# Kernel tuning notes

Hardware: AMD Instinct MI355X
Metric: run time of the kernel (lower is better)

## Reference

```python
import jax, jax.numpy as jnp
import numpy as np

B, H, W = 8, 160, 160
L = H * W  # 25600, matches nn.LayerNorm(25600)
QDIM = KDIM = MID = OUT = 256
HEADS = 8
HEAD_DIM = MID // HEADS  # 32
LN_EPS = 1e-5


def conv1x1(x, w, b):
    # x: [N,C,H,W], w: [O,C], b: [O] -> [N,O,H,W]
    return jnp.einsum('nchw,oc->nohw', x, w) + b[None, :, None, None]


def setup_inputs() -> dict:
    key = jax.random.key(0)
    ks = jax.random.split(key, 12)
    s = 0.02
    return {
        'query': jax.random.normal(ks[0], (B, QDIM, H, W), jnp.float32),
        'key': jax.random.normal(ks[1], (B, KDIM, H, W), jnp.float32),
        'Wq': jax.random.normal(ks[2], (MID, QDIM), jnp.float32) * s,
        'bq': jnp.zeros((MID,), jnp.float32),
        'Wk': jax.random.normal(ks[3], (MID, KDIM), jnp.float32) * s,
        'bk': jnp.zeros((MID,), jnp.float32),
        'Wv': jax.random.normal(ks[4], (MID, KDIM), jnp.float32) * s,
        'bv': jnp.zeros((MID,), jnp.float32),
        'Wo': jax.random.normal(ks[5], (OUT, MID), jnp.float32) * s,
        'bo': jnp.zeros((OUT,), jnp.float32),
        'gamma': jnp.ones((L,), jnp.float32),
        'beta': jnp.zeros((L,), jnp.float32),
    }


def reference(query, key, Wq, bq, Wk, bk, Wv, bv, Wo, bo, gamma, beta):
    # 1x1-conv projections, flatten spatial dims to L
    q = conv1x1(query, Wq, bq).reshape(B, HEADS, HEAD_DIM, L)
    k = conv1x1(key, Wk, bk).reshape(B, HEADS, HEAD_DIM, L)
    v = conv1x1(key, Wv, bv).reshape(B, HEADS, HEAD_DIM, L)
    # NOTE: faithful to the source, scores contract over L (spatial), giving
    # a [B, heads, head_dim, head_dim] channel-attention matrix.
    scores = jnp.einsum('nhdl,nhel->nhde', q, k) / (KDIM ** 0.5)
    attn = jax.nn.softmax(scores, axis=-1)  # dropout is identity at eval
    out = jnp.einsum('nhde,nhel->nhdl', attn, v).reshape(B, MID, L)
    # LayerNorm over the flattened spatial axis (size 25600)
    mu = jnp.mean(out, axis=-1, keepdims=True)
    var = jnp.var(out, axis=-1, keepdims=True)
    out = (out - mu) * jax.lax.rsqrt(var + LN_EPS) * gamma + beta
    out = out.reshape(B, MID, H, W)
    return conv1x1(out, Wo, bo)
```

## Files before the change

### kernel.cpp

```cpp
#include <hip/hip_runtime.h>
#include <hip/hip_bf16.h>
#include <stdint.h>

#define LROW 25600
#define NCH 256
#define LN_EPS 1e-5f

typedef float f32x4 __attribute__((ext_vector_type(4)));
typedef __bf16 bf16x8 __attribute__((ext_vector_type(8)));

__device__ __forceinline__ bf16x8 cvt8(f32x4 a, f32x4 b) {
  bf16x8 r;
  r[0] = (__bf16)a[0]; r[1] = (__bf16)a[1]; r[2] = (__bf16)a[2]; r[3] = (__bf16)a[3];
  r[4] = (__bf16)b[0]; r[5] = (__bf16)b[1]; r[6] = (__bf16)b[2]; r[7] = (__bf16)b[3];
  return r;
}

__device__ __forceinline__ void wg_bar() {
  asm volatile("s_waitcnt lgkmcnt(0)\n\ts_barrier" ::: "memory");
}

__global__ __launch_bounds__(1024, 4) void gram_k(
    const float* __restrict__ qg, const float* __restrict__ kg,
    float* __restrict__ Gd, float* __restrict__ Gkkd,
    float* __restrict__ sq, float* __restrict__ sk) {
  __shared__ __align__(16) __bf16 lA[256 * 32];
  __shared__ __align__(16) __bf16 lB[256 * 32];

  const int bid = blockIdx.x;
  const int x = bid & 7;
  int n = bid >> 3;
  int b = 0, s = 0;
  for (int bb = 0; bb < 8; ++bb) {
    const int gsl = (x - bb) & 7;
    const int gs = (21 * gsl + 7) >> 3, ge = (21 * gsl + 28) >> 3;
    const int ks = (11 * gsl + 7) >> 3, ke = (11 * gsl + 18) >> 3;
    const int cnt = (ge - gs) + (ke - ks);
    if (n < cnt) {
      b = bb;
      s = (n < ge - gs) ? (gs + n) : (21 + ks + (n - (ge - gs)));
      break;
    }
    n -= cnt;
  }

  const int mat = (s < 21) ? 0 : 1;
  const int idx = mat ? (s - 21) : s;
  const int parts = mat ? 11 : 21;
  const int c0 = (800 * idx) / parts, c1 = (800 * (idx + 1)) / parts;
  const int nc = c1 - c0;
  const int tid = threadIdx.x;
  const int w = tid >> 6, lane = tid & 63;
  const int wr = w >> 2, wc = w & 3;
  const int lr = lane & 15, g = lane >> 4;
  const float* Ag = (mat ? kg : qg) + (size_t)b * NCH * LROW;
  const float* Bg = kg + (size_t)b * NCH * LROW;

  const int rowS = tid >> 2, uS = tid & 3;
  const int uSw = uS ^ ((rowS >> 1) & 3);
  const size_t gOff = (size_t)rowS * LROW + uS * 8;
  __bf16* ldsA_dst = lA + rowS * 32 + uSw * 8;
  __bf16* ldsB_dst = lB + rowS * 32 + uSw * 8;

  const f32x4 zero = {0.f, 0.f, 0.f, 0.f};
  f32x4 acc[4][4];
#pragma unroll
  for (int i = 0; i < 4; ++i)
#pragma unroll
    for (int j = 0; j < 4; ++j) acc[i][j] = zero;

  float rsum = 0.f;

  auto LOADG = [&](int c, f32x4* d) {
    const float* pa = Ag + gOff + (size_t)c * 32;
    d[0] = *(const f32x4*)pa;
    d[1] = *(const f32x4*)(pa + 4);
    if (mat == 0) {
      const float* pb = Bg + gOff + (size_t)c * 32;
      d[2] = *(const f32x4*)pb;
      d[3] = *(const f32x4*)(pb + 4);
    }
  };

  auto PROCESS = [&](f32x4* d) {
#pragma unroll
    for (int e = 0; e < 4; ++e) rsum += d[0][e] + d[1][e];
    *(bf16x8*)ldsA_dst = cvt8(d[0], d[1]);
    if (mat == 0) *(bf16x8*)ldsB_dst = cvt8(d[2], d[3]);
    wg_bar();
    const __bf16* Bp = mat ? lA : lB;
    bf16x8 af[4];
#pragma unroll
    for (int i = 0; i < 4; ++i) {
      const int row = wr * 64 + i * 16 + lr;
      const int u = g ^ ((row >> 1) & 3);
      af[i] = *(const bf16x8*)(lA + row * 32 + u * 8);
    }
#pragma unroll
    for (int j = 0; j < 4; ++j) {
      const int row = wc * 64 + j * 16 + lr;
      const int u = g ^ ((row >> 1) & 3);
      bf16x8 bfj = *(const bf16x8*)(Bp + row * 32 + u * 8);
#pragma unroll
      for (int i = 0; i < 4; ++i)
        acc[i][j] = __builtin_amdgcn_mfma_f32_16x16x32_bf16(af[i], bfj, acc[i][j], 0, 0, 0);
    }
    wg_bar();
  };

  f32x4 bA[4], bB[4];
  LOADG(c0, bA);
  int cc = 0;
  for (; cc + 2 <= nc; cc += 2) {
    LOADG(c0 + cc + 1, bB);
    PROCESS(bA);
    if (cc + 2 < nc) LOADG(c0 + cc + 2, bA);
    PROCESS(bB);
  }
  if (cc < nc) PROCESS(bA);

  atomicAdd((mat ? sk : sq) + b * NCH + rowS, rsum);

  float* Gout = (mat ? Gkkd : Gd) + (size_t)b * 65536;
#pragma unroll
  for (int i = 0; i < 4; ++i)
#pragma unroll
    for (int j = 0; j < 4; ++j) {
      const int col = wc * 64 + j * 16 + lr;
      const int row0 = wr * 64 + i * 16 + g * 4;
#pragma unroll
      for (int r = 0; r < 4; ++r)
        atomicAdd(&Gout[(size_t)(row0 + r) * NCH + col], acc[i][j][r]);
    }
}

__global__ __launch_bounds__(256) void attn_k(
    const float* __restrict__ G, const float* __restrict__ sq,
    const float* __restrict__ sk,
    const float* __restrict__ Wq, const float* __restrict__ bq,
    const float* __restrict__ Wk, const float* __restrict__ bk,
    const float* __restrict__ Wv, const float* __restrict__ bv,
    float* __restrict__ M, float* __restrict__ cvec) {
  __shared__ float Wql[32][257];
  __shared__ float Wkl[32][257];
  __shared__ float QGl[32][257];
  __shared__ float Sl[32][33];
  __shared__ float Al[32][33];
  __shared__ float ul[32], wl[32];
  const int b = blockIdx.x >> 3, h = blockIdx.x & 7;
  const int t = threadIdx.x;
  const float* Gb = G + (size_t)b * 65536;

  for (int i = 0; i < 32; ++i) {
    int idx = i * 256 + t;
    int d = idx >> 8, c = idx & 255;
    Wql[d][c] = Wq[(h * 32 + d) * 256 + c];
    Wkl[d][c] = Wk[(h * 32 + d) * 256 + c];
  }
  __syncthreads();
  {
    float a[32];
#pragma unroll
    for (int d = 0; d < 32; ++d) a[d] = 0.f;
    for (int c = 0; c < 256; ++c) {
      float gv = Gb[c * 256 + t];
#pragma unroll
      for (int d = 0; d < 32; ++d) a[d] += Wql[d][c] * gv;
    }
    for (int d = 0; d < 32; ++d) QGl[d][t] = a[d];
  }
  if (t < 32) {
    float u = 0.f, wv = 0.f;
    for (int c = 0; c < 256; ++c) {
      u += Wql[t][c] * sq[b * 256 + c];
      wv += Wkl[t][c] * sk[b * 256 + c];
    }
    ul[t] = u; wl[t] = wv;
  }
  __syncthreads();
  for (int i = 0; i < 4; ++i) {
    int idx = i * 256 + t;
    int d = idx >> 5, e = idx & 31;
    float sv = 0.f;
    for (int c = 0; c < 256; ++c) sv += QGl[d][c] * Wkl[e][c];
    float bqd = bq[h * 32 + d], bke = bk[h * 32 + e];
    Sl[d][e] = (sv + ul[d] * bke + bqd * wl[e] + 25600.f * bqd * bke) * (1.f / 16.f);
  }
  __syncthreads();
  if (t < 32) {
    float m = -1e30f;
    for (int e = 0; e < 32; ++e) m = fmaxf(m, Sl[t][e]);
    float ssum = 0.f;
    for (int e = 0; e < 32; ++e) { float p = __expf(Sl[t][e] - m); Al[t][e] = p; ssum += p; }
    float is = 1.f / ssum;
    for (int e = 0; e < 32; ++e) Al[t][e] *= is;
  }
  __syncthreads();
  {
    float a[32];
#pragma unroll
    for (int d = 0; d < 32; ++d) a[d] = 0.f;
    for (int e = 0; e < 32; ++e) {
      float wv = Wv[(h * 32 + e) * 256 + t];
#pragma unroll
      for (int d = 0; d < 32; ++d) a[d] += Al[d][e] * wv;
    }
    for (int d = 0; d < 32; ++d) M[((size_t)b * 256 + h * 32 + d) * 256 + t] = a[d];
  }
  if (t < 32) {
    float cv = 0.f;
    for (int e = 0; e < 32; ++e) cv += Al[t][e] * bv[h * 32 + e];
    cvec[b * 256 + h * 32 + t] = cv;
  }
}

__global__ __launch_bounds__(256) void stats_k(
    const float* __restrict__ Gkk, const float* __restrict__ M,
    const float* __restrict__ sk, const float* __restrict__ cvec,
    float* __restrict__ mu, float* __restrict__ inv) {
  __shared__ float Ml[32][257];
  __shared__ float Ql[32][257];
  const int b = blockIdx.x >> 3, cb = blockIdx.x & 7;
  const int t = threadIdx.x;
  const float* Gk = Gkk + (size_t)b * 65536;
  for (int i = 0; i < 32; ++i) {
    int idx = i * 256 + t;
    Ml[idx >> 8][idx & 255] = M[((size_t)b * 256 + cb * 32 + (idx >> 8)) * 256 + (idx & 255)];
  }
  __syncthreads();
  {
    float a[32];
#pragma unroll
    for (int c = 0; c < 32; ++c) a[c] = 0.f;
    for (int cc = 0; cc < 256; ++cc) {
      float gv = Gk[cc * 256 + t];
#pragma unroll
      for (int c = 0; c < 32; ++c) a[c] += Ml[c][cc] * gv;
    }
    for (int c = 0; c < 32; ++c) Ql[c][t] = a[c];
  }
  __syncthreads();
  if (t < 32) {
    float qf = 0.f, msk = 0.f;
    for (int j = 0; j < 256; ++j) {
      qf += Ql[t][j] * Ml[t][j];
      msk += Ml[t][j] * sk[b * 256 + j];
    }
    int c = cb * 32 + t;
    float cv = cvec[b * 256 + c];
    float muv = msk * (1.f / 25600.f) + cv;
    float sum2 = qf + 2.f * cv * msk + 25600.f * cv * cv;
    float var = sum2 * (1.f / 25600.f) - muv * muv;
    mu[b * 256 + c] = muv;
    inv[b * 256 + c] = rsqrtf(var + LN_EPS);
  }
}

__global__ __launch_bounds__(256) void pmat_k(
    const float* __restrict__ M, const float* __restrict__ Wo,
    const float* __restrict__ inv, const float* __restrict__ cvec,
    const float* __restrict__ mu, __bf16* __restrict__ Pb,
    float* __restrict__ t1, float* __restrict__ wsum) {
  __shared__ float Wol[32][257];
  __shared__ float invl[256];
  const int b = blockIdx.x >> 3, ob = blockIdx.x & 7;
  const int t = threadIdx.x;
  invl[t] = inv[b * 256 + t];
  __syncthreads();
  for (int i = 0; i < 32; ++i) {
    int idx = i * 256 + t;
    int o = idx >> 8, c = idx & 255;
    Wol[o][c] = Wo[(ob * 32 + o) * 256 + c] * invl[c];
  }
  __syncthreads();
  {
    float a[32];
#pragma unroll
    for (int o = 0; o < 32; ++o) a[o] = 0.f;
    for (int c = 0; c < 256; ++c) {
      float m = M[((size_t)b * 256 + c) * 256 + t];
#pragma unroll
      for (int o = 0; o < 32; ++o) a[o] += Wol[o][c] * m;
    }
    for (int o = 0; o < 32; ++o)
      Pb[((size_t)b * 256 + ob * 32 + o) * 256 + t] = (__bf16)a[o];
  }
  if (t < 32) {
    float s1 = 0.f, s2 = 0.f;
    for (int c = 0; c < 256; ++c) {
      s1 += Wol[t][c] * (cvec[b * 256 + c] - mu[b * 256 + c]);
      s2 += Wo[(ob * 32 + t) * 256 + c];
    }
    t1[b * 256 + ob * 32 + t] = s1;
    wsum[b * 256 + ob * 32 + t] = s2;
  }
}

__global__ __launch_bounds__(512, 4) void outf_k(
    const float* __restrict__ key, const __bf16* __restrict__ Pb,
    const float* __restrict__ t1, const float* __restrict__ wsum,
    const float* __restrict__ bo, const float* __restrict__ gamma,
    const float* __restrict__ beta, float* __restrict__ out) {
  __shared__ __align__(16) __bf16 Bt[128 * 256];
  const int bid = blockIdx.x;
  const int b = bid / 200, lt = bid % 200, l0 = lt * 128;
  const int tid = threadIdx.x, w = tid >> 6, lane = tid & 63;
  const int wr = w >> 1, wc = w & 1;
  const int lr = lane & 15, g = lane >> 4;
  const float* Kb = key + (size_t)b * NCH * LROW;

  {
    const int c = tid & 255, seg = tid >> 8;
    const int uc = c >> 3, cb2 = (c & 7) * 2;
    const float* src = Kb + (size_t)c * LROW + l0 + seg * 64;
#pragma unroll
    for (int i = 0; i < 16; ++i) {
      f32x4 v = *(const f32x4*)(src + i * 4);
#pragma unroll
      for (int j = 0; j < 4; ++j) {
        const int l = seg * 64 + i * 4 + j;
        *(__bf16*)((char*)Bt + l * 512 + ((uc ^ (l & 7)) << 4) + cb2) = (__bf16)v[j];
      }
    }
  }
  __syncthreads();

  const f32x4 zero = {0.f, 0.f, 0.f, 0.f};
  f32x4 acc[4][4];
#pragma unroll
  for (int i = 0; i < 4; ++i)
#pragma unroll
    for (int j = 0; j < 4; ++j) acc[i][j] = zero;

  const __bf16* Pbase = Pb + (size_t)b * 65536;
#pragma unroll
  for (int ks = 0; ks < 8; ++ks) {
    bf16x8 af[4];
#pragma unroll
    for (int i = 0; i < 4; ++i) {
      const int row = wr * 64 + i * 16 + lr;
      af[i] = *(const bf16x8*)(Pbase + (size_t)row * 256 + ks * 32 + g * 8);
    }
#pragma unroll
    for (int j = 0; j < 4; ++j) {
      const int col = wc * 64 + j * 16 + lr;
      const int unit = ks * 4 + g;
      bf16x8 bfj = *(const bf16x8*)((const char*)Bt + col * 512 + ((unit ^ (col & 7)) << 4));
#pragma unroll
      for (int i = 0; i < 4; ++i)
        acc[i][j] = __builtin_amdgcn_mfma_f32_16x16x32_bf16(af[i], bfj, acc[i][j], 0, 0, 0);
    }
  }

  float t1r[4][4], wsr[4][4], bor[4][4];
#pragma unroll
  for (int i = 0; i < 4; ++i)
#pragma unroll
    for (int r = 0; r < 4; ++r) {
      const int row = wr * 64 + i * 16 + g * 4 + r;
      t1r[i][r] = t1[b * 256 + row];
      wsr[i][r] = wsum[b * 256 + row];
      bor[i][r] = bo[row];
    }
#pragma unroll
  for (int j = 0; j < 4; ++j) {
    const int colg = l0 + wc * 64 + j * 16 + lr;
    const float gm = gamma[colg];
    const float bt = beta[colg];
#pragma unroll
    for (int i = 0; i < 4; ++i) {
      const int row0 = wr * 64 + i * 16 + g * 4;
#pragma unroll
      for (int r = 0; r < 4; ++r) {
        const int row = row0 + r;
        float v = gm * (acc[i][j][r] + t1r[i][r]) + bt * wsr[i][r] + bor[i][r];
        out[((size_t)b * 256 + row) * LROW + colg] = v;
      }
    }
  }
}

extern "C" void kernel_launch(void* const* d_in, const int* in_sizes, int n_in,
                              void* d_out, int out_size, void* d_ws, size_t ws_size,
                              hipStream_t stream) {
  const float* query = (const float*)d_in[0];
  const float* key   = (const float*)d_in[1];
  const float* Wq = (const float*)d_in[2];
  const float* bq = (const float*)d_in[3];
  const float* Wk = (const float*)d_in[4];
  const float* bk = (const float*)d_in[5];
  const float* Wv = (const float*)d_in[6];
  const float* bv = (const float*)d_in[7];
  const float* Wo = (const float*)d_in[8];
  const float* bo = (const float*)d_in[9];
  const float* gamma = (const float*)d_in[10];
  const float* beta  = (const float*)d_in[11];
  float* out = (float*)d_out;

  float* ws = (float*)d_ws;
  float* G    = ws;
  float* Gkk  = G + 524288;
  float* sq   = Gkk + 524288;
  float* sk   = sq + 2048;
  float* M    = sk + 2048;
  float* cvec = M + 524288;
  float* mu   = cvec + 2048;
  float* inv  = mu + 2048;
  float* t1   = inv + 2048;
  float* wsum = t1 + 2048;
  __bf16* Pb  = (__bf16*)(wsum + 2048);

  hipMemsetAsync(d_ws, 0, (size_t)(524288 * 2 + 4096) * sizeof(float), stream);

  gram_k<<<256, 1024, 0, stream>>>(query, key, G, Gkk, sq, sk);
  attn_k<<<64, 256, 0, stream>>>(G, sq, sk, Wq, bq, Wk, bk, Wv, bv, M, cvec);
  stats_k<<<64, 256, 0, stream>>>(Gkk, M, sk, cvec, mu, inv);
  pmat_k<<<64, 256, 0, stream>>>(M, Wo, inv, cvec, mu, Pb, t1, wsum);
  outf_k<<<1600, 512, 0, stream>>>(key, Pb, t1, wsum, bo, gamma, beta, out);
}
```

Measured before the change: 707.1 us.

## Retile Gram kernel into 128x128 double-buffered tiles with split-K partials and reduction

Changes the Gram computation from 256 blocks of 1024 threads covering a full 256x256 tile to 768 blocks of 256 threads. Each block computes a 128x128 quadrant over one of 12 K-slices and double-buffers shared memory, which removes one barrier per step. When the workspace is large enough, partial Gram matrices are written out plainly and summed by a new reduce kernel, replacing the global float atomics. It also adds unroll pragmas to the small attention and stats kernels, reorders the output kernel's block-to-batch mapping, and restructures its epilogue. In exchange the partial buffers cost extra memory traffic, and the Kkt Gram is now computed in full rather than reusing the symmetric load.

Result: slower. 1.032 ms (+46.0%).

```diff
diff --git a/kernel.cpp b/kernel.cpp
--- a/kernel.cpp
+++ b/kernel.cpp
@@ -20,47 +20,39 @@
   asm volatile("s_waitcnt lgkmcnt(0)\n\ts_barrier" ::: "memory");
 }
 
-__global__ __launch_bounds__(1024, 4) void gram_k(
+template <int FULL>
+__global__ __launch_bounds__(256, 3) void gram_k(
     const float* __restrict__ qg, const float* __restrict__ kg,
-    float* __restrict__ Gd, float* __restrict__ Gkkd,
+    float* __restrict__ P0,
+    float* __restrict__ P1,
     float* __restrict__ sq, float* __restrict__ sk) {
-  __shared__ __align__(16) __bf16 lA[256 * 32];
-  __shared__ __align__(16) __bf16 lB[256 * 32];
+  __shared__ __align__(16) __bf16 lA[2][128 * 32];
+  __shared__ __align__(16) __bf16 lB[2][128 * 32];
 
   const int bid = blockIdx.x;
-  const int x = bid & 7;
-  int n = bid >> 3;
-  int b = 0, s = 0;
-  for (int bb = 0; bb < 8; ++bb) {
-    const int gsl = (x - bb) & 7;
-    const int gs = (21 * gsl + 7) >> 3, ge = (21 * gsl + 28) >> 3;
-    const int ks = (11 * gsl + 7) >> 3, ke = (11 * gsl + 18) >> 3;
-    const int cnt = (ge - gs) + (ke - ks);
-    if (n < cnt) {
-      b = bb;
-      s = (n < ge - gs) ? (gs + n) : (21 + ks + (n - (ge - gs)));
-      break;
-    }
-    n -= cnt;
-  }
-
-  const int mat = (s < 21) ? 0 : 1;
-  const int idx = mat ? (s - 21) : s;
-  const int parts = mat ? 11 : 21;
-  const int c0 = (800 * idx) / parts, c1 = (800 * (idx + 1)) / parts;
+  const int xcd = bid & 7, s2 = bid >> 3;
+  const int tile = s2 & 7, gslot = s2 >> 3;
+  const int g = gslot * 8 + xcd;
+  const int b = g / 12, ks = g % 12;
+  const int mat = tile >> 2;
+  const int ri = (tile >> 1) & 1, ci = tile & 1;
+  const int c0 = (800 * ks) / 12, c1 = (800 * (ks + 1)) / 12;
   const int nc = c1 - c0;
+
   const int tid = threadIdx.x;
   const int w = tid >> 6, lane = tid & 63;
-  const int wr = w >> 2, wc = w & 3;
-  const int lr = lane & 15, g = lane >> 4;
-  const float* Ag = (mat ? kg : qg) + (size_t)b * NCH * LROW;
-  const float* Bg = kg + (size_t)b * NCH * LROW;
-
-  const int rowS = tid >> 2, uS = tid & 3;
-  const int uSw = uS ^ ((rowS >> 1) & 3);
-  const size_t gOff = (size_t)rowS * LROW + uS * 8;
-  __bf16* ldsA_dst = lA + rowS * 32 + uSw * 8;
-  __bf16* ldsB_dst = lB + rowS * 32 + uSw * 8;
+  const int wr = w >> 1, wc = w & 1;
+  const int lr = lane & 15, gq = lane >> 4;
+
+  const float* Abase = (mat ? kg : qg) + (size_t)b * NCH * LROW + (size_t)(ri * 128) * LROW;
+  const float* Bbase = kg + (size_t)b * NCH * LROW + (size_t)(ci * 128) * LROW;
+
+  const int rowS = tid >> 1, h = tid & 1;
+  const float* Ap = Abase + (size_t)rowS * LROW + h * 16 + (size_t)c0 * 32;
+  const float* Bp = Bbase + (size_t)rowS * LROW + h * 16 + (size_t)c0 * 32;
+  const int swz = rowS & 3;
+  const int d0 = rowS * 32 + (((2 * h) ^ swz) * 8);
+  const int d1 = rowS * 32 + (((2 * h + 1) ^ swz) * 8);
 
   const f32x4 zero = {0.f, 0.f, 0.f, 0.f};
   f32x4 acc[4][4];
@@ -70,68 +62,101 @@
     for (int j = 0; j < 4; ++j) acc[i][j] = zero;
 
   float rsum = 0.f;
+  f32x4 bA[8], bB[8];
 
   auto LOADG = [&](int c, f32x4* d) {
-    const float* pa = Ag + gOff + (size_t)c * 32;
-    d[0] = *(const f32x4*)pa;
-    d[1] = *(const f32x4*)(pa + 4);
-    if (mat == 0) {
-      const float* pb = Bg + gOff + (size_t)c * 32;
-      d[2] = *(const f32x4*)pb;
-      d[3] = *(const f32x4*)(pb + 4);
-    }
+    const float* pa = Ap + (size_t)c * 32;
+#pragma unroll
+    for (int i = 0; i < 4; ++i) d[i] = *(const f32x4*)(pa + i * 4);
+    const float* pb = Bp + (size_t)c * 32;
+#pragma unroll
+    for (int i = 0; i < 4; ++i) d[4 + i] = *(const f32x4*)(pb + i * 4);
   };
-
-  auto PROCESS = [&](f32x4* d) {
-#pragma unroll
-    for (int e = 0; e < 4; ++e) rsum += d[0][e] + d[1][e];
-    *(bf16x8*)ldsA_dst = cvt8(d[0], d[1]);
-    if (mat == 0) *(bf16x8*)ldsB_dst = cvt8(d[2], d[3]);
-    wg_bar();
-    const __bf16* Bp = mat ? lA : lB;
+  auto WRITE = [&](f32x4* d, int buf) {
+#pragma unroll
+    for (int e = 0; e < 4; ++e)
+      rsum += d[0][e] + d[1][e] + d[2][e] + d[3][e];
+    *(bf16x8*)(&lA[buf][d0]) = cvt8(d[0], d[1]);
+    *(bf16x8*)(&lA[buf][d1]) = cvt8(d[2], d[3]);
+    *(bf16x8*)(&lB[buf][d0]) = cvt8(d[4], d[5]);
+    *(bf16x8*)(&lB[buf][d1]) = cvt8(d[6], d[7]);
+  };
+  auto COMPUTE = [&](int buf) {
     bf16x8 af[4];
 #pragma unroll
     for (int i = 0; i < 4; ++i) {
       const int row = wr * 64 + i * 16 + lr;
-      const int u = g ^ ((row >> 1) & 3);
-      af[i] = *(const bf16x8*)(lA + row * 32 + u * 8);
+      af[i] = *(const bf16x8*)(&lA[buf][row * 32 + ((gq ^ (row & 3)) * 8)]);
     }
 #pragma unroll
     for (int j = 0; j < 4; ++j) {
       const int row = wc * 64 + j * 16 + lr;
-      const int u = g ^ ((row >> 1) & 3);
-      bf16x8 bfj = *(const bf16x8*)(Bp + row * 32 + u * 8);
+      bf16x8 bfj = *(const bf16x8*)(&lB[buf][row * 32 + ((gq ^ (row & 3)) * 8)]);
 #pragma unroll
       for (int i = 0; i < 4; ++i)
         acc[i][j] = __builtin_amdgcn_mfma_f32_16x16x32_bf16(af[i], bfj, acc[i][j], 0, 0, 0);
     }
-    wg_bar();
   };
 
-  f32x4 bA[4], bB[4];
-  LOADG(c0, bA);
+  LOADG(0, bA);
+  LOADG(1, bB);
   int cc = 0;
   for (; cc + 2 <= nc; cc += 2) {
-    LOADG(c0 + cc + 1, bB);
-    PROCESS(bA);
-    if (cc + 2 < nc) LOADG(c0 + cc + 2, bA);
-    PROCESS(bB);
-  }
-  if (cc < nc) PROCESS(bA);
-
-  atomicAdd((mat ? sk : sq) + b * NCH + rowS, rsum);
-
-  float* Gout = (mat ? Gkkd : Gd) + (size_t)b * 65536;
-#pragma unroll
-  for (int i = 0; i < 4; ++i)
-#pragma unroll
-    for (int j = 0; j < 4; ++j) {
-      const int col = wc * 64 + j * 16 + lr;
-      const int row0 = wr * 64 + i * 16 + g * 4;
-#pragma unroll
-      for (int r = 0; r < 4; ++r)
-        atomicAdd(&Gout[(size_t)(row0 + r) * NCH + col], acc[i][j][r]);
-    }
+    WRITE(bA, 0);
+    wg_bar();
+    if (cc + 2 < nc) LOADG(cc + 2, bA);
+    COMPUTE(0);
+    WRITE(bB, 1);
+    wg_bar();
+    if (cc + 3 < nc) LOADG(cc + 3, bB);
+    COMPUTE(1);
+  }
+  if (cc < nc) { WRITE(bA, 0); wg_bar(); COMPUTE(0); }
+
+  rsum += __shfl_xor(rsum, 1);
+  if (h == 0 && ci == 0)
+    atomicAdd((mat ? sk : sq) + b * NCH + ri * 128 + rowS, rsum);
+
+  if (FULL) {
+    float* Gout = P0 + ((size_t)(b * 12 + ks) * 2 + mat) * 65536;
+#pragma unroll
+    for (int i = 0; i < 4; ++i)
+#pragma unroll
+      for (int r = 0; r < 4; ++r) {
+        const int rr = ri * 128 + wr * 64 + i * 16 + gq * 4 + r;
+#pragma unroll
+        for (int j = 0; j < 4; ++j) {
+          const int col = ci * 128 + wc * 64 + j * 16 + lr;
+          Gout[(size_t)rr * 256 + col] = acc[i][j][r];
+        }
+      }
+  } else {
+    float* Gout = (mat ? P1 : P0) + (size_t)b * 65536;
+#pragma unroll
+    for (int i = 0; i < 4; ++i)
+#pragma unroll
+      for (int r = 0; r < 4; ++r) {
+        const int rr = ri * 128 + wr * 64 + i * 16 + gq * 4 + r;
+#pragma unroll
+        for (int j = 0; j < 4; ++j) {
+          const int col = ci * 128 + wc * 64 + j * 16 + lr;
+          atomicAdd(&Gout[(size_t)rr * 256 + col], acc[i][j][r]);
+        }
+      }
+  }
+}
+
+__global__ __launch_bounds__(256) void reduce_k(
+    const float* __restrict__ Pp, float* __restrict__ G, float* __restrict__ Gkk) {
+  const int f = (blockIdx.x * 256 + threadIdx.x) * 4;
+  const int b = f >> 17, rem = f & 131071;
+  const int mat = rem >> 16, r = rem & 65535;
+  f32x4 a = {0.f, 0.f, 0.f, 0.f};
+#pragma unroll
+  for (int ks = 0; ks < 12; ++ks)
+    a += *(const f32x4*)(Pp + ((size_t)(b * 12 + ks) * 2 + mat) * 65536 + r);
+  float* dst = (mat ? Gkk : G) + (size_t)b * 65536 + r;
+  *(f32x4*)dst = a;
 }
 
 __global__ __launch_bounds__(256) void attn_k(
@@ -147,21 +172,22 @@
   __shared__ float Sl[32][33];
   __shared__ float Al[32][33];
   __shared__ float ul[32], wl[32];
-  const int b = blockIdx.x >> 3, h = blockIdx.x & 7;
+  const int b = blockIdx.x >> 3, hh = blockIdx.x & 7;
   const int t = threadIdx.x;
   const float* Gb = G + (size_t)b * 65536;
 
   for (int i = 0; i < 32; ++i) {
     int idx = i * 256 + t;
     int d = idx >> 8, c = idx & 255;
-    Wql[d][c] = Wq[(h * 32 + d) * 256 + c];
-    Wkl[d][c] = Wk[(h * 32 + d) * 256 + c];
+    Wql[d][c] = Wq[(hh * 32 + d) * 256 + c];
+    Wkl[d][c] = Wk[(hh * 32 + d) * 256 + c];
   }
   __syncthreads();
   {
     float a[32];
 #pragma unroll
     for (int d = 0; d < 32; ++d) a[d] = 0.f;
+#pragma unroll 8
     for (int c = 0; c < 256; ++c) {
       float gv = Gb[c * 256 + t];
 #pragma unroll
@@ -171,6 +197,7 @@
   }
   if (t < 32) {
     float u = 0.f, wv = 0.f;
+#pragma unroll 8
     for (int c = 0; c < 256; ++c) {
       u += Wql[t][c] * sq[b * 256 + c];
       wv += Wkl[t][c] * sk[b * 256 + c];
@@ -182,8 +209,9 @@
     int idx = i * 256 + t;
     int d = idx >> 5, e = idx & 31;
     float sv = 0.f;
+#pragma unroll 8
     for (int c = 0; c < 256; ++c) sv += QGl[d][c] * Wkl[e][c];
-    float bqd = bq[h * 32 + d], bke = bk[h * 32 + e];
+    float bqd = bq[hh * 32 + d], bke = bk[hh * 32 + e];
     Sl[d][e] = (sv + ul[d] * bke + bqd * wl[e] + 25600.f * bqd * bke) * (1.f / 16.f);
   }
   __syncthreads();
@@ -191,7 +219,7 @@
     float m = -1e30f;
     for (int e = 0; e < 32; ++e) m = fmaxf(m, Sl[t][e]);
     float ssum = 0.f;
-    for (int e = 0; e < 32; ++e) { float p = __expf(Sl[t][e] - m); Al[t][e] = p; ssum += p; }
+    for (int e = 0; e < 32; ++e) { float pp = __expf(Sl[t][e] - m); Al[t][e] = pp; ssum += pp; }
     float is = 1.f / ssum;
     for (int e = 0; e < 32; ++e) Al[t][e] *= is;
   }
@@ -200,17 +228,18 @@
     float a[32];
 #pragma unroll
     for (int d = 0; d < 32; ++d) a[d] = 0.f;
+#pragma unroll 4
     for (int e = 0; e < 32; ++e) {
-      float wv = Wv[(h * 32 + e) * 256 + t];
+      float wv = Wv[(hh * 32 + e) * 256 + t];
 #pragma unroll
       for (int d = 0; d < 32; ++d) a[d] += Al[d][e] * wv;
     }
-    for (int d = 0; d < 32; ++d) M[((size_t)b * 256 + h * 32 + d) * 256 + t] = a[d];
+    for (int d = 0; d < 32; ++d) M[((size_t)b * 256 + hh * 32 + d) * 256 + t] = a[d];
   }
   if (t < 32) {
     float cv = 0.f;
-    for (int e = 0; e < 32; ++e) cv += Al[t][e] * bv[h * 32 + e];
-    cvec[b * 256 + h * 32 + t] = cv;
+    for (int e = 0; e < 32; ++e) cv += Al[t][e] * bv[hh * 32 + e];
+    cvec[b * 256 + hh * 32 + t] = cv;
   }
 }
 
@@ -232,6 +261,7 @@
     float a[32];
 #pragma unroll
     for (int c = 0; c < 32; ++c) a[c] = 0.f;
+#pragma unroll 8
     for (int cc = 0; cc < 256; ++cc) {
       float gv = Gk[cc * 256 + t];
 #pragma unroll
@@ -242,6 +272,7 @@
   __syncthreads();
   if (t < 32) {
     float qf = 0.f, msk = 0.f;
+#pragma unroll 8
     for (int j = 0; j < 256; ++j) {
       qf += Ql[t][j] * Ml[t][j];
       msk += Ml[t][j] * sk[b * 256 + j];
@@ -277,6 +308,7 @@
     float a[32];
 #pragma unroll
     for (int o = 0; o < 32; ++o) a[o] = 0.f;
+#pragma unroll 8
     for (int c = 0; c < 256; ++c) {
       float m = M[((size_t)b * 256 + c) * 256 + t];
 #pragma unroll
@@ -287,6 +319,7 @@
   }
   if (t < 32) {
     float s1 = 0.f, s2 = 0.f;
+#pragma unroll 8
     for (int c = 0; c < 256; ++c) {
       s1 += Wol[t][c] * (cvec[b * 256 + c] - mu[b * 256 + c]);
       s2 += Wo[(ob * 32 + t) * 256 + c];
@@ -303,7 +336,7 @@
     const float* __restrict__ beta, float* __restrict__ out) {
   __shared__ __align__(16) __bf16 Bt[128 * 256];
   const int bid = blockIdx.x;
-  const int b = bid / 200, lt = bid % 200, l0 = lt * 128;
+  const int b = bid & 7, lt = bid >> 3, l0 = lt * 128;
   const int tid = threadIdx.x, w = tid >> 6, lane = tid & 63;
   const int wr = w >> 1, wc = w & 1;
   const int lr = lane & 15, g = lane >> 4;
@@ -352,32 +385,21 @@
     }
   }
 
-  float t1r[4][4], wsr[4][4], bor[4][4];
 #pragma unroll
   for (int i = 0; i < 4; ++i)
 #pragma unroll
     for (int r = 0; r < 4; ++r) {
       const int row = wr * 64 + i * 16 + g * 4 + r;
-      t1r[i][r] = t1[b * 256 + row];
-      wsr[i][r] = wsum[b * 256 + row];
-      bor[i][r] = bo[row];
-    }
-#pragma unroll
-  for (int j = 0; j < 4; ++j) {
-    const int colg = l0 + wc * 64 + j * 16 + lr;
-    const float gm = gamma[colg];
-    const float bt = beta[colg];
-#pragma unroll
-    for (int i = 0; i < 4; ++i) {
-      const int row0 = wr * 64 + i * 16 + g * 4;
-#pragma unroll
-      for (int r = 0; r < 4; ++r) {
-        const int row = row0 + r;
-        float v = gm * (acc[i][j][r] + t1r[i][r]) + bt * wsr[i][r] + bor[i][r];
-        out[((size_t)b * 256 + row) * LROW + colg] = v;
+      const float t1v = t1[b * 256 + row];
+      const float wsv = wsum[b * 256 + row];
+      const float bov = bo[row];
+      const size_t ro = ((size_t)b * 256 + row) * LROW + l0;
+#pragma unroll
+      for (int j = 0; j < 4; ++j) {
+        const int cl = wc * 64 + j * 16 + lr;
+        out[ro + cl] = gamma[l0 + cl] * (acc[i][j][r] + t1v) + beta[l0 + cl] * wsv + bov;
       }
     }
-  }
 }
 
 extern "C" void kernel_launch(void* const* d_in, const int* in_sizes, int n_in,
@@ -409,10 +431,17 @@
   float* t1   = inv + 2048;
   float* wsum = t1 + 2048;
   __bf16* Pb  = (__bf16*)(wsum + 2048);
-
-  hipMemsetAsync(d_ws, 0, (size_t)(524288 * 2 + 4096) * sizeof(float), stream);
-
-  gram_k<<<256, 1024, 0, stream>>>(query, key, G, Gkk, sq, sk);
+  float* Pp = ws + 1849344;
+  const size_t need = (size_t)(1849344 + 12582912) * 4;
+
+  if (ws_size >= need) {
+    hipMemsetAsync(sq, 0, 4096 * sizeof(float), stream);
+    gram_k<1><<<768, 256, 0, stream>>>(query, key, Pp, nullptr, sq, sk);
+    reduce_k<<<1024, 256, 0, stream>>>(Pp, G, Gkk);
+  } else {
+    hipMemsetAsync(d_ws, 0, (size_t)1052672 * sizeof(float), stream);
+    gram_k<0><<<768, 256, 0, stream>>>(query, key, G, Gkk, sq, sk);
+  }
   attn_k<<<64, 256, 0, stream>>>(G, sq, sk, Wq, bq, Wk, bk, Wv, bv, M, cvec);
   stats_k<<<64, 256, 0, stream>>>(Gkk, M, sk, cvec, mu, inv);
   pmat_k<<<64, 256, 0, stream>>>(M, Wo, inv, cvec, mu, Pb, t1, wsum);
```
